# Kernel optimization log

Measured on AMD Instinct MI355X. Metric: run time of the kernel, lower is better.

## Reference

```python
import jax, jax.numpy as jnp
import numpy as np

N = 100000      # nodes
E = 1600000     # message-passing edges
P = 1000000     # prediction edges
DIN = 128       # node_in_channels
H = 128         # hidden_channels
DOUT = 64       # out_channels (node embedding)
EIN = 32        # edge_in_channels
EPS = 1e-5


def setup_inputs() -> dict:
    key = jax.random.key(0)
    ks = iter(jax.random.split(key, 48))
    nk = lambda: next(ks)
    rn = lambda shape: jax.random.normal(nk(), shape, dtype=jnp.float32)
    glorot = lambda shape: rn(shape) * (1.0 / np.sqrt(shape[-1]))
    inp = {
        "x": rn((N, DIN)),
        "edge_index": jax.random.randint(nk(), (2, E), 0, N),
        "pred_edge_index": jax.random.randint(nk(), (2, P), 0, N),
        "edge_features": rn((P, EIN)),
        # SAGEConv layer 1: lin_l (aggregated, with bias), lin_r (root, no bias)
        "sage1_Wl": glorot((H, DIN)), "sage1_bl": jnp.zeros((H,), jnp.float32), "sage1_Wr": glorot((H, DIN)),
        "bn1_g": jnp.ones((H,), jnp.float32), "bn1_b": jnp.zeros((H,), jnp.float32),
        "bn1_m": rn((H,)) * 0.1, "bn1_v": jnp.ones((H,), jnp.float32),
        # SAGEConv layer 2
        "sage2_Wl": glorot((DOUT, H)), "sage2_bl": jnp.zeros((DOUT,), jnp.float32), "sage2_Wr": glorot((DOUT, H)),
        # edge MLP: Linear(EIN, H//2) -> BN -> ReLU -> Linear(H//2, H//4)
        "edge_W1": glorot((H // 2, EIN)), "edge_b1": jnp.zeros((H // 2,), jnp.float32),
        "ebn_g": jnp.ones((H // 2,), jnp.float32), "ebn_b": jnp.zeros((H // 2,), jnp.float32),
        "ebn_m": rn((H // 2,)) * 0.1, "ebn_v": jnp.ones((H // 2,), jnp.float32),
        "edge_W2": glorot((H // 4, H // 2)), "edge_b2": jnp.zeros((H // 4,), jnp.float32),
        # predictor: Linear(2*DOUT+H//4, H) -> BN -> ReLU -> Linear(H, H//2) -> BN -> ReLU -> Linear(H//2, 1)
        "p_W1": glorot((H, 2 * DOUT + H // 4)), "p_b1": jnp.zeros((H,), jnp.float32),
        "pbn1_g": jnp.ones((H,), jnp.float32), "pbn1_b": jnp.zeros((H,), jnp.float32),
        "pbn1_m": rn((H,)) * 0.1, "pbn1_v": jnp.ones((H,), jnp.float32),
        "p_W2": glorot((H // 2, H)), "p_b2": jnp.zeros((H // 2,), jnp.float32),
        "pbn2_g": jnp.ones((H // 2,), jnp.float32), "pbn2_b": jnp.zeros((H // 2,), jnp.float32),
        "pbn2_m": rn((H // 2,)) * 0.1, "pbn2_v": jnp.ones((H // 2,), jnp.float32),
        "p_W3": glorot((1, H // 2)), "p_b3": jnp.zeros((1,), jnp.float32),
    }
    return inp


def _bn(h, g, b, m, v):
    # eval-mode BatchNorm1d with running stats
    return (h - m) * (g / jnp.sqrt(v + EPS)) + b


def _sage(h, src, dst, Wl, bl, Wr):
    # PyG SAGEConv (mean aggr): lin_l(mean of h[src] at dst) + lin_r(h)
    msg = jax.ops.segment_sum(h[src], dst, num_segments=N)        # [N, d]
    cnt = jax.ops.segment_sum(jnp.ones((src.shape[0],), h.dtype), dst, num_segments=N)
    agg = msg / jnp.maximum(cnt, 1.0)[:, None]
    return agg @ Wl.T + bl + h @ Wr.T


def reference(x, edge_index, pred_edge_index, edge_features,
              sage1_Wl, sage1_bl, sage1_Wr, bn1_g, bn1_b, bn1_m, bn1_v,
              sage2_Wl, sage2_bl, sage2_Wr,
              edge_W1, edge_b1, ebn_g, ebn_b, ebn_m, ebn_v, edge_W2, edge_b2,
              p_W1, p_b1, pbn1_g, pbn1_b, pbn1_m, pbn1_v,
              p_W2, p_b2, pbn2_g, pbn2_b, pbn2_m, pbn2_v, p_W3, p_b3):
    src, dst = edge_index[0], edge_index[1]
    # GraphSAGE encoder (eval mode: dropout off, BN running stats)
    h = _sage(x, src, dst, sage1_Wl, sage1_bl, sage1_Wr)
    h = jax.nn.relu(_bn(h, bn1_g, bn1_b, bn1_m, bn1_v))
    z = _sage(h, src, dst, sage2_Wl, sage2_bl, sage2_Wr)          # [N, DOUT]
    # edge-pair gather + concat
    combined = jnp.concatenate([z[pred_edge_index[0]], z[pred_edge_index[1]]], axis=-1)  # [P, 2*DOUT]
    # edge feature MLP
    e = edge_features @ edge_W1.T + edge_b1
    e = jax.nn.relu(_bn(e, ebn_g, ebn_b, ebn_m, ebn_v))
    e = e @ edge_W2.T + edge_b2                                   # [P, H//4]
    combined = jnp.concatenate([combined, e], axis=-1)            # [P, 2*DOUT + H//4]
    # predictor MLP
    u = combined @ p_W1.T + p_b1
    u = jax.nn.relu(_bn(u, pbn1_g, pbn1_b, pbn1_m, pbn1_v))
    u = u @ p_W2.T + p_b2
    u = jax.nn.relu(_bn(u, pbn2_g, pbn2_b, pbn2_m, pbn2_v))
    out = u @ p_W3.T + p_b3                                       # [P, 1]
    return out[:, 0]
```

## Files before the change

kernel.cpp:

```cpp
#include <hip/hip_runtime.h>

#define Nn 100000
#define Ee 1600000
#define Pp 1000000
#define EPSf 1e-5f

typedef _Float16 f16x8 __attribute__((ext_vector_type(8)));
typedef _Float16 f16x4 __attribute__((ext_vector_type(4)));
typedef _Float16 f16x2 __attribute__((ext_vector_type(2)));
typedef float f32x4 __attribute__((ext_vector_type(4)));

__device__ __forceinline__ float4 ld4(const float* p) { return *(const float4*)p; }

#define oW1l 0
#define oW1r 16384
#define oW2l 32768
#define oW2r 40960
#define oW1a 49152
#define oW1b 57344
#define oW1c 65536
#define oWe1 69632
#define oWe2 71680
#define oWp2 73728
#define W16_TOTAL 81920

#define BN_TOTAL 608

#define BSH 9
#define NB2 196
#define SCAP2 9216
#define ECHUNK 4096
#define NCHUNK ((Ee + ECHUNK - 1) / ECHUNK)

__global__ __launch_bounds__(256) void prep_kernel(
    const float* __restrict__ x,
    const float* __restrict__ s1Wl, const float* __restrict__ s1Wr,
    const float* __restrict__ s2Wl, const float* __restrict__ s2Wr,
    const float* __restrict__ pW1,  const float* __restrict__ eW1,
    const float* __restrict__ eW2,  const float* __restrict__ pW2,
    const float* __restrict__ eb1,
    const float* __restrict__ ebng, const float* __restrict__ ebnb,
    const float* __restrict__ ebnm, const float* __restrict__ ebnv,
    const float* __restrict__ eb2,
    const float* __restrict__ pb1,
    const float* __restrict__ p1g, const float* __restrict__ p1b,
    const float* __restrict__ p1m, const float* __restrict__ p1v,
    const float* __restrict__ pb2,
    const float* __restrict__ p2g, const float* __restrict__ p2b,
    const float* __restrict__ p2m, const float* __restrict__ p2v,
    const float* __restrict__ pW3,
    _Float16* __restrict__ w16, float* __restrict__ bnA,
    _Float16* __restrict__ x16) {
    int tid = blockIdx.x * 256 + threadIdx.x;
    if (tid < W16_TOTAL) {
        float v;
        if (tid < 16384)      v = s1Wl[tid];
        else if (tid < 32768) v = s1Wr[tid - 16384];
        else if (tid < 40960) v = s2Wl[tid - 32768];
        else if (tid < 49152) v = s2Wr[tid - 40960];
        else if (tid < 57344) { int l = tid - 49152; v = pW1[(l >> 6) * 160 + (l & 63)]; }
        else if (tid < 65536) { int l = tid - 57344; v = pW1[(l >> 6) * 160 + 64 + (l & 63)]; }
        else if (tid < 69632) { int l = tid - 65536; v = pW1[(l >> 5) * 160 + 128 + (l & 31)]; }
        else if (tid < 71680) v = eW1[tid - 69632];
        else if (tid < 73728) v = eW2[tid - 71680];
        else                  v = pW2[tid - 73728];
        w16[tid] = (_Float16)v;
    } else if (tid < W16_TOTAL + BN_TOTAL) {
        int b = tid - W16_TOTAL;
        float v;
        if (b < 64)       v = ebng[b] * rsqrtf(ebnv[b] + EPSf);
        else if (b < 128) { int c = b - 64;  float s = ebng[c] * rsqrtf(ebnv[c] + EPSf);
                            v = (eb1[c] - ebnm[c]) * s + ebnb[c]; }
        else if (b < 256) { int c = b - 128; v = p1g[c] * rsqrtf(p1v[c] + EPSf); }
        else if (b < 384) { int c = b - 256; float s = p1g[c] * rsqrtf(p1v[c] + EPSf);
                            v = (pb1[c] - p1m[c]) * s + p1b[c]; }
        else if (b < 448) { int c = b - 384; v = p2g[c] * rsqrtf(p2v[c] + EPSf); }
        else if (b < 512) { int c = b - 448; float s = p2g[c] * rsqrtf(p2v[c] + EPSf);
                            v = (pb2[c] - p2m[c]) * s + p2b[c]; }
        else if (b < 544) v = eb2[b - 512];
        else              v = pW3[b - 544];
        bnA[b] = v;
    }
    int stride = gridDim.x * 256;
    const int NV = Nn * 128 / 4;
    for (int i = tid; i < NV; i += stride) {
        float4 v = ((const float4*)x)[i];
        f16x4 h = {(_Float16)v.x, (_Float16)v.y, (_Float16)v.z, (_Float16)v.w};
        ((f16x4*)x16)[i] = h;
    }
}

__global__ __launch_bounds__(256) void bucketA_kernel(
    const int* __restrict__ src, const int* __restrict__ dst,
    unsigned* __restrict__ stage, unsigned* __restrict__ gcur) {
    __shared__ unsigned hist[NB2];
    __shared__ unsigned base[NB2];
    const int t = threadIdx.x;
    const int e0 = blockIdx.x * ECHUNK;
    for (int u = t; u < NB2; u += 256) hist[u] = 0u;
    __syncthreads();

    int sv[16], dv[16];
#pragma unroll
    for (int k = 0; k < 16; ++k) {
        int e = e0 + k * 256 + t;
        if (e < Ee) {
            sv[k] = src[e];
            dv[k] = dst[e];
            atomicAdd(&hist[dv[k] >> BSH], 1u);
        } else dv[k] = -1;
    }
    __syncthreads();
    for (int u = t; u < NB2; u += 256) {
        unsigned h = hist[u];
        base[u] = h ? atomicAdd(&gcur[u], h) : 0u;
        hist[u] = 0u;
    }
    __syncthreads();
#pragma unroll
    for (int k = 0; k < 16; ++k) {
        if (dv[k] >= 0) {
            int b = dv[k] >> BSH;
            unsigned p = atomicAdd(&hist[b], 1u);
            stage[(size_t)b * SCAP2 + base[b] + p] =
                ((unsigned)sv[k] << BSH) | (unsigned)(dv[k] & 511);
        }
    }
}

__global__ __launch_bounds__(256) void countC_kernel(
    const unsigned* __restrict__ stage, const unsigned* __restrict__ gcur,
    unsigned* __restrict__ deg) {
    __shared__ unsigned cnt[512];
    const int b = blockIdx.x;
    const int t = threadIdx.x;
    cnt[t] = 0u; cnt[t + 256] = 0u;
    __syncthreads();
    unsigned m = gcur[b];
    const unsigned* sp = stage + (size_t)b * SCAP2;
    for (unsigned i = t; i < m; i += 256)
        atomicAdd(&cnt[sp[i] & 511], 1u);
    __syncthreads();
    int n0 = b << BSH;
    if (n0 + t < Nn)       deg[n0 + t] = cnt[t];
    if (n0 + 256 + t < Nn) deg[n0 + 256 + t] = cnt[t + 256];
}

__global__ __launch_bounds__(1024) void scanA_kernel(const unsigned* __restrict__ deg,
                                                     unsigned* __restrict__ escan,
                                                     unsigned* __restrict__ bsum) {
    __shared__ unsigned s[1024];
    int t = threadIdx.x;
    int gid = blockIdx.x * 1024 + t;
    unsigned v = (gid < Nn) ? deg[gid] : 0u;
    s[t] = v;
    __syncthreads();
    for (int off = 1; off < 1024; off <<= 1) {
        unsigned u = (t >= off) ? s[t - off] : 0u;
        __syncthreads();
        s[t] += u;
        __syncthreads();
    }
    if (gid < Nn) escan[gid] = s[t] - v;
    if (t == 1023) bsum[blockIdx.x] = s[1023];
}

__global__ __launch_bounds__(128) void scanB_kernel(const unsigned* __restrict__ bsum,
                                                    unsigned* __restrict__ boff,
                                                    int nblk) {
    __shared__ unsigned s[128];
    int t = threadIdx.x;
    unsigned v = (t < nblk) ? bsum[t] : 0u;
    s[t] = v;
    __syncthreads();
    for (int off = 1; off < 128; off <<= 1) {
        unsigned u = (t >= off) ? s[t - off] : 0u;
        __syncthreads();
        s[t] += u;
        __syncthreads();
    }
    if (t < nblk) boff[t] = s[t] - v;
}

__global__ __launch_bounds__(1024) void scanC_kernel(const unsigned* __restrict__ escan,
                                                     const unsigned* __restrict__ boff,
                                                     int* __restrict__ rowptr) {
    int t = threadIdx.x;
    int gid = blockIdx.x * 1024 + t;
    if (gid < Nn) rowptr[gid] = (int)(escan[gid] + boff[blockIdx.x]);
    if (gid == 0) rowptr[Nn] = Ee;
}

__global__ __launch_bounds__(256) void scatterE_kernel(
    const unsigned* __restrict__ stage, const unsigned* __restrict__ gcur,
    const int* __restrict__ rowptr, int* __restrict__ elist) {
    __shared__ int lbase[512];
    __shared__ unsigned cur[512];
    const int b = blockIdx.x;
    const int t = threadIdx.x;
    const int n0 = b << BSH;
    lbase[t]       = (n0 + t < Nn)       ? rowptr[n0 + t]       : 0;
    lbase[t + 256] = (n0 + 256 + t < Nn) ? rowptr[n0 + 256 + t] : 0;
    cur[t] = 0u; cur[t + 256] = 0u;
    __syncthreads();
    unsigned m = gcur[b];
    const unsigned* sp = stage + (size_t)b * SCAP2;
    for (unsigned i = t; i < m; i += 256) {
        unsigned v = sp[i];
        int lid = v & 511;
        unsigned p = atomicAdd(&cur[lid], 1u);
        elist[lbase[lid] + p] = (int)(v >> BSH);
    }
}

template<int W>
__global__ __launch_bounds__(256, 8) void aggregate16_kernel(
    const _Float16* __restrict__ feat,
    const int* __restrict__ rowptr,
    const int* __restrict__ elist,
    _Float16* __restrict__ outp) {
    int node = (blockIdx.x * 256 + threadIdx.x) >> 6;
    int lane = threadIdx.x & 63;
    if (node >= Nn) return;
    constexpr int SEGS = W / 8;
    constexpr int RPI  = 64 / SEGS;
    const int r = lane / SEGS, c = lane % SEGS;
    int beg = rowptr[node], end = rowptr[node + 1];
    int n = end - beg;
    float acc[8];
#pragma unroll
    for (int k = 0; k < 8; ++k) acc[k] = 0.f;
    for (int c0 = 0; c0 < n; c0 += 64) {
        int m = min(64, n - c0);
        int se = (lane < m) ? elist[beg + c0 + lane] : 0;
        int iters = (m + RPI - 1) / RPI;
#pragma unroll 2
        for (int i = 0; i < iters; ++i) {
            int j = i * RPI + r;
            int s = __shfl(se, j);
            if (j < m) {
                f16x8 v = *(const f16x8*)(feat + (size_t)s * W + c * 8);
#pragma unroll
                for (int k = 0; k < 8; ++k) acc[k] += (float)v[k];
            }
        }
    }
#pragma unroll
    for (int k = 0; k < 8; ++k) {
#pragma unroll
        for (int off = SEGS; off < 64; off <<= 1)
            acc[k] += __shfl_xor(acc[k], off);
    }
    if (r == 0) {
        float inv = 1.0f / fmaxf((float)n, 1.0f);
        f16x8 o;
#pragma unroll
        for (int k = 0; k < 8; ++k) o[k] = (_Float16)(acc[k] * inv);
        *(f16x8*)(outp + (size_t)node * W + c * 8) = o;
    }
}

__global__ __launch_bounds__(256) void dense1_kernel(
    const _Float16* __restrict__ A1, const _Float16* __restrict__ A2,
    const _Float16* __restrict__ W1, const _Float16* __restrict__ W2,
    const float* __restrict__ lb,
    const float* __restrict__ bng, const float* __restrict__ bnb,
    const float* __restrict__ bnm, const float* __restrict__ bnv,
    _Float16* __restrict__ out) {
    const int t = threadIdx.x;
    const int w = t >> 6, lane = t & 63;
    const int lrow = lane & 15, lq = lane >> 4;
    const int row0 = blockIdx.x * 64 + w * 16;
    const int ld = min(row0 + lrow, Nn - 1);

    f16x8 a1[4], a2[4];
#pragma unroll
    for (int i = 0; i < 4; ++i) {
        a1[i] = *(const f16x8*)(A1 + (size_t)ld * 128 + i * 32 + lq * 8);
        a2[i] = *(const f16x8*)(A2 + (size_t)ld * 128 + i * 32 + lq * 8);
    }
#pragma unroll
    for (int nt = 0; nt < 8; ++nt) {
        const _Float16* w1r = W1 + (size_t)(nt * 16 + lrow) * 128;
        const _Float16* w2r = W2 + (size_t)(nt * 16 + lrow) * 128;
        f32x4 c = {0.f, 0.f, 0.f, 0.f};
#pragma unroll
        for (int i = 0; i < 4; ++i) {
            c = __builtin_amdgcn_mfma_f32_16x16x32_f16(a1[i], *(const f16x8*)(w1r + i * 32 + lq * 8), c, 0, 0, 0);
            c = __builtin_amdgcn_mfma_f32_16x16x32_f16(a2[i], *(const f16x8*)(w2r + i * 32 + lq * 8), c, 0, 0, 0);
        }
        int cc = nt * 16 + lrow;
        float s = bng[cc] * rsqrtf(bnv[cc] + EPSf);
        float h = (lb[cc] - bnm[cc]) * s + bnb[cc];
#pragma unroll
        for (int r = 0; r < 4; ++r) {
            int gr = row0 + lq * 4 + r;
            if (gr < Nn)
                out[(size_t)gr * 128 + cc] = (_Float16)fmaxf(c[r] * s + h, 0.f);
        }
    }
}

__global__ __launch_bounds__(256) void gemmY_kernel(
    const _Float16* __restrict__ A, const _Float16* __restrict__ W,
    _Float16* __restrict__ out) {
    const int t = threadIdx.x;
    const int w = t >> 6, lane = t & 63;
    const int lrow = lane & 15, lq = lane >> 4;
    const int row0 = blockIdx.x * 64 + w * 16;
    const int ld = min(row0 + lrow, Nn - 1);
    f16x8 a[4];
#pragma unroll
    for (int i = 0; i < 4; ++i)
        a[i] = *(const f16x8*)(A + (size_t)ld * 128 + i * 32 + lq * 8);
#pragma unroll
    for (int nt = 0; nt < 4; ++nt) {
        const _Float16* wr = W + (size_t)(nt * 16 + lrow) * 128;
        f32x4 c = {0.f, 0.f, 0.f, 0.f};
#pragma unroll
        for (int i = 0; i < 4; ++i)
            c = __builtin_amdgcn_mfma_f32_16x16x32_f16(a[i], *(const f16x8*)(wr + i * 32 + lq * 8), c, 0, 0, 0);
        int cc = nt * 16 + lrow;
#pragma unroll
        for (int r = 0; r < 4; ++r) {
            int gr = row0 + lq * 4 + r;
            if (gr < Nn) out[(size_t)gr * 64 + cc] = (_Float16)c[r];
        }
    }
}

__global__ __launch_bounds__(256) void dense2b_kernel(
    const _Float16* __restrict__ aggY, const _Float16* __restrict__ A2,
    const _Float16* __restrict__ W2, const float* __restrict__ lb,
    _Float16* __restrict__ out) {
    const int t = threadIdx.x;
    const int w = t >> 6, lane = t & 63;
    const int lrow = lane & 15, lq = lane >> 4;
    const int row0 = blockIdx.x * 64 + w * 16;
    const int ld = min(row0 + lrow, Nn - 1);
    f16x8 a[4];
#pragma unroll
    for (int i = 0; i < 4; ++i)
        a[i] = *(const f16x8*)(A2 + (size_t)ld * 128 + i * 32 + lq * 8);
#pragma unroll
    for (int nt = 0; nt < 4; ++nt) {
        const _Float16* wr = W2 + (size_t)(nt * 16 + lrow) * 128;
        f32x4 c = {0.f, 0.f, 0.f, 0.f};
#pragma unroll
        for (int i = 0; i < 4; ++i)
            c = __builtin_amdgcn_mfma_f32_16x16x32_f16(a[i], *(const f16x8*)(wr + i * 32 + lq * 8), c, 0, 0, 0);
        int cc = nt * 16 + lrow;
        float b = lb[cc];
#pragma unroll
        for (int r = 0; r < 4; ++r) {
            int gr = row0 + lq * 4 + r;
            if (gr < Nn) {
                float g = (float)aggY[(size_t)gr * 64 + cc];
                out[(size_t)gr * 64 + cc] = (_Float16)(c[r] + g + b);
            }
        }
    }
}

__global__ __launch_bounds__(256) void emlp_kernel(
    const float* __restrict__ ef,
    const _Float16* __restrict__ w16,
    const float* __restrict__ bnA,
    _Float16* __restrict__ e2out) {
    __shared__ __align__(16) _Float16 E1[64 * 72];
    const int t = threadIdx.x;
    const int lane = t & 63, w = t >> 6;
    const int lrow = lane & 15, lq = lane >> 4;
    const int e0 = blockIdx.x * 64 + w * 16;
    const int erow = w * 16 + lrow;

    const float* src = ef + (size_t)(e0 + lrow) * 32 + lq * 8;
    float4 f0 = ld4(src), f1 = ld4(src + 4);
    f16x8 bf = {(_Float16)f0.x, (_Float16)f0.y, (_Float16)f0.z, (_Float16)f0.w,
                (_Float16)f1.x, (_Float16)f1.y, (_Float16)f1.z, (_Float16)f1.w};

#pragma unroll
    for (int nt = 0; nt < 4; ++nt) {
        f16x8 wf = *(const f16x8*)(w16 + oWe1 + (nt * 16 + lrow) * 32 + lq * 8);
        f32x4 c = {0.f, 0.f, 0.f, 0.f};
        c = __builtin_amdgcn_mfma_f32_16x16x32_f16(wf, bf, c, 0, 0, 0);
        int cb = nt * 16 + lq * 4;
        float4 s = *(const float4*)(bnA + cb);
        float4 h = *(const float4*)(bnA + 64 + cb);
        f16x4 o;
        o[0] = (_Float16)fmaxf(c[0] * s.x + h.x, 0.f);
        o[1] = (_Float16)fmaxf(c[1] * s.y + h.y, 0.f);
        o[2] = (_Float16)fmaxf(c[2] * s.z + h.z, 0.f);
        o[3] = (_Float16)fmaxf(c[3] * s.w + h.w, 0.f);
        *(f16x4*)(E1 + erow * 72 + cb) = o;
    }
    f16x8 a0 = *(const f16x8*)(E1 + erow * 72 + lq * 8);
    f16x8 a1 = *(const f16x8*)(E1 + erow * 72 + 32 + lq * 8);
#pragma unroll
    for (int nt = 0; nt < 2; ++nt) {
        f16x8 b0 = *(const f16x8*)(w16 + oWe2 + (nt * 16 + lrow) * 64 + lq * 8);
        f16x8 b1 = *(const f16x8*)(w16 + oWe2 + (nt * 16 + lrow) * 64 + 32 + lq * 8);
        f32x4 c = {0.f, 0.f, 0.f, 0.f};
        c = __builtin_amdgcn_mfma_f32_16x16x32_f16(b0, a0, c, 0, 0, 0);
        c = __builtin_amdgcn_mfma_f32_16x16x32_f16(b1, a1, c, 0, 0, 0);
        int cb = nt * 16 + lq * 4;
        float4 bias = *(const float4*)(bnA + 512 + cb);
        f16x4 o;
        o[0] = (_Float16)(c[0] + bias.x);
        o[1] = (_Float16)(c[1] + bias.y);
        o[2] = (_Float16)(c[2] + bias.z);
        o[3] = (_Float16)(c[3] + bias.w);
        *(f16x4*)(e2out + (size_t)(e0 + lrow) * 32 + cb) = o;
    }
}

#define EPB 256
#define NT  ((Pp + EPB - 1) / EPB)
#define EGRID 256

#define oL_W1a 0
#define oL_W1b 18432
#define oL_W1c 36864
#define oL_Wp2 47104
#define oL_BN  64512
#define oL_ZU  66304
#define SMEM_BYTES 135936

__global__ __launch_bounds__(1024, 4) void edge_kernel(
    const int* __restrict__ pe,
    const _Float16* __restrict__ e2,
    const _Float16* __restrict__ z,
    const _Float16* __restrict__ w16,
    const float* __restrict__ bnA,
    const float* __restrict__ pb3,
    float* __restrict__ out) {
    __shared__ __align__(16) unsigned char smem[SMEM_BYTES];
    _Float16* LW1a = (_Float16*)(smem + oL_W1a);
    _Float16* LW1b = (_Float16*)(smem + oL_W1b);
    _Float16* LW1c = (_Float16*)(smem + oL_W1c);
    _Float16* LWp2 = (_Float16*)(smem + oL_Wp2);
    float*    LBN  = (float*)(smem + oL_BN);
    _Float16* ZU   = (_Float16*)(smem + oL_ZU);

    const float* bn2s = LBN;        const float* bn2h = LBN + 128;
    const float* bn3s = LBN + 256;  const float* bn3h = LBN + 320;
    const float* wp3g = LBN + 384;

    const int t = threadIdx.x;
    const int lane = t & 63;
    const int w = t >> 6;
    const int m0 = w * 16;
    const int lrow = lane & 15;
    const int lq = lane >> 4;
    const float pb3v = pb3[0];

    auto load_idx = [&](int tl, int& ia, int& ib) {
        int e = min(tl * EPB + m0 + lrow, Pp - 1);
        ia = pe[e];
        ib = pe[Pp + e];
    };
    auto gather = [&](int tl, int ia, int ib, f16x8* F) {
        F[0] = *(const f16x8*)(z + (size_t)ia * 64 + lq * 8);
        F[1] = *(const f16x8*)(z + (size_t)ia * 64 + 32 + lq * 8);
        F[2] = *(const f16x8*)(z + (size_t)ib * 64 + lq * 8);
        F[3] = *(const f16x8*)(z + (size_t)ib * 64 + 32 + lq * 8);
        int e = min(tl * EPB + m0 + lrow, Pp - 1);
        F[4] = *(const f16x8*)(e2 + (size_t)e * 32 + lq * 8);
    };

    int tile = blockIdx.x;
    int ia1, ib1;
    {
        int ia0, ib0;
        load_idx(tile, ia0, ib0);
        load_idx(tile + EGRID, ia1, ib1);
        f16x8 F[5];
        gather(tile, ia0, ib0, F);

        { int r = t >> 3, s = t & 7;
          *(f16x8*)(LW1a + r * 72 + s * 8) = *(const f16x8*)(w16 + oW1a + r * 64 + s * 8);
          *(f16x8*)(LW1b + r * 72 + s * 8) = *(const f16x8*)(w16 + oW1b + r * 64 + s * 8); }
        if (t < 512) { int r = t >> 2, s = t & 3;
          *(f16x8*)(LW1c + r * 40 + s * 8) = *(const f16x8*)(w16 + oW1c + r * 32 + s * 8); }
        { int r = t >> 4, s = t & 15;
          *(f16x8*)(LWp2 + r * 136 + s * 8) = *(const f16x8*)(w16 + oWp2 + r * 128 + s * 8); }
        if (t < 384) LBN[t] = bnA[128 + t];
        else if (t < 448) LBN[t] = bnA[544 + (t - 384)];
        __syncthreads();

        const int erow = m0 + lrow;
        const int zr = erow * 136;
        for (; tile < NT; tile += EGRID) {
            f16x8 G[5];
            gather(tile + EGRID, ia1, ib1, G);
            int ia2, ib2;
            load_idx(tile + 2 * EGRID, ia2, ib2);

            const bool act = (tile * EPB + m0) < Pp;
            if (act) {
                __builtin_amdgcn_s_setprio(1);
#pragma unroll
                for (int nt = 0; nt < 8; ++nt) {
                    const _Float16* wa = LW1a + (nt * 16 + lrow) * 72;
                    const _Float16* wb = LW1b + (nt * 16 + lrow) * 72;
                    const _Float16* wc = LW1c + (nt * 16 + lrow) * 40;
                    f32x4 c = {0.f, 0.f, 0.f, 0.f};
                    c = __builtin_amdgcn_mfma_f32_16x16x32_f16(*(const f16x8*)(wa + lq * 8),      F[0], c, 0, 0, 0);
                    c = __builtin_amdgcn_mfma_f32_16x16x32_f16(*(const f16x8*)(wa + 32 + lq * 8), F[1], c, 0, 0, 0);
                    c = __builtin_amdgcn_mfma_f32_16x16x32_f16(*(const f16x8*)(wb + lq * 8),      F[2], c, 0, 0, 0);
                    c = __builtin_amdgcn_mfma_f32_16x16x32_f16(*(const f16x8*)(wb + 32 + lq * 8), F[3], c, 0, 0, 0);
                    c = __builtin_amdgcn_mfma_f32_16x16x32_f16(*(const f16x8*)(wc + lq * 8),      F[4], c, 0, 0, 0);
                    int cb = nt * 16 + lq * 4;
                    float4 s = *(const float4*)(bn2s + cb);
                    float4 h = *(const float4*)(bn2h + cb);
                    f16x4 o;
                    o[0] = (_Float16)fmaxf(c[0] * s.x + h.x, 0.f);
                    o[1] = (_Float16)fmaxf(c[1] * s.y + h.y, 0.f);
                    o[2] = (_Float16)fmaxf(c[2] * s.z + h.z, 0.f);
                    o[3] = (_Float16)fmaxf(c[3] * s.w + h.w, 0.f);
                    *(f16x4*)(ZU + zr + cb) = o;
                }
                __builtin_amdgcn_s_setprio(0);
                {
                    f16x8 a0 = *(const f16x8*)(ZU + zr + 0  + lq * 8);
                    f16x8 a1 = *(const f16x8*)(ZU + zr + 32 + lq * 8);
                    f16x8 a2 = *(const f16x8*)(ZU + zr + 64 + lq * 8);
                    f16x8 a3 = *(const f16x8*)(ZU + zr + 96 + lq * 8);
                    float acc = 0.f;
                    __builtin_amdgcn_s_setprio(1);
#pragma unroll
                    for (int nt = 0; nt < 4; ++nt) {
                        const _Float16* wr = LWp2 + (nt * 16 + lrow) * 136 + lq * 8;
                        f32x4 c = {0.f, 0.f, 0.f, 0.f};
                        c = __builtin_amdgcn_mfma_f32_16x16x32_f16(*(const f16x8*)(wr + 0),  a0, c, 0, 0, 0);
                        c = __builtin_amdgcn_mfma_f32_16x16x32_f16(*(const f16x8*)(wr + 32), a1, c, 0, 0, 0);
                        c = __builtin_amdgcn_mfma_f32_16x16x32_f16(*(const f16x8*)(wr + 64), a2, c, 0, 0, 0);
                        c = __builtin_amdgcn_mfma_f32_16x16x32_f16(*(const f16x8*)(wr + 96), a3, c, 0, 0, 0);
                        int cb = nt * 16 + lq * 4;
                        float4 s  = *(const float4*)(bn3s + cb);
                        float4 h  = *(const float4*)(bn3h + cb);
                        float4 w3 = *(const float4*)(wp3g + cb);
                        acc += fmaxf(c[0] * s.x + h.x, 0.f) * w3.x;
                        acc += fmaxf(c[1] * s.y + h.y, 0.f) * w3.y;
                        acc += fmaxf(c[2] * s.z + h.z, 0.f) * w3.z;
                        acc += fmaxf(c[3] * s.w + h.w, 0.f) * w3.w;
                    }
                    __builtin_amdgcn_s_setprio(0);
                    acc += __shfl_xor(acc, 16);
                    acc += __shfl_xor(acc, 32);
                    if (lane < 16) out[tile * EPB + m0 + lane] = acc + pb3v;
                }
            }
#pragma unroll
            for (int i = 0; i < 5; ++i) F[i] = G[i];
            ia1 = ia2; ib1 = ib2;
        }
    }
}

extern "C" void kernel_launch(void* const* d_in, const int* in_sizes, int n_in,
                              void* d_out, int out_size, void* d_ws, size_t ws_size,
                              hipStream_t stream) {
    const float* x    = (const float*)d_in[0];
    const int*   eidx = (const int*)d_in[1];
    const int*   pe   = (const int*)d_in[2];
    const float* ef   = (const float*)d_in[3];
    const float* s1Wl = (const float*)d_in[4];
    const float* s1bl = (const float*)d_in[5];
    const float* s1Wr = (const float*)d_in[6];
    const float* bn1g = (const float*)d_in[7];
    const float* bn1b = (const float*)d_in[8];
    const float* bn1m = (const float*)d_in[9];
    const float* bn1v = (const float*)d_in[10];
    const float* s2Wl = (const float*)d_in[11];
    const float* s2bl = (const float*)d_in[12];
    const float* s2Wr = (const float*)d_in[13];
    const float* eW1  = (const float*)d_in[14];
    const float* eb1  = (const float*)d_in[15];
    const float* ebng = (const float*)d_in[16];
    const float* ebnb = (const float*)d_in[17];
    const float* ebnm = (const float*)d_in[18];
    const float* ebnv = (const float*)d_in[19];
    const float* eW2  = (const float*)d_in[20];
    const float* eb2  = (const float*)d_in[21];
    const float* pW1  = (const float*)d_in[22];
    const float* pb1  = (const float*)d_in[23];
    const float* p1g  = (const float*)d_in[24];
    const float* p1b  = (const float*)d_in[25];
    const float* p1m  = (const float*)d_in[26];
    const float* p1v  = (const float*)d_in[27];
    const float* pW2  = (const float*)d_in[28];
    const float* pb2  = (const float*)d_in[29];
    const float* p2g  = (const float*)d_in[30];
    const float* p2b  = (const float*)d_in[31];
    const float* p2m  = (const float*)d_in[32];
    const float* p2v  = (const float*)d_in[33];
    const float* pW3  = (const float*)d_in[34];
    const float* pb3  = (const float*)d_in[35];
    float* out = (float*)d_out;

    char* wk = (char*)d_ws;
    auto carve = [&](size_t bytes) {
        char* p = wk;
        wk += (bytes + 255) & ~(size_t)255;
        return p;
    };
    unsigned*  deg    = (unsigned*)carve((size_t)Nn * 4);
    unsigned*  gcur   = (unsigned*)carve((size_t)256 * 4);
    int*       rowptr = (int*)carve((size_t)(Nn + 1) * 4);
    int*       elist  = (int*)carve((size_t)Ee * 4);
    unsigned*  escan  = (unsigned*)carve((size_t)Nn * 4);
    unsigned*  bsum   = (unsigned*)carve(128 * 4);
    unsigned*  boff   = (unsigned*)carve(128 * 4);
    _Float16*  w16    = (_Float16*)carve((size_t)W16_TOTAL * 2);
    float*     bnA    = (float*)carve((size_t)BN_TOTAL * 4);
    _Float16*  bufX   = (_Float16*)carve((size_t)Nn * 128 * 2);
    _Float16*  bufA   = (_Float16*)carve((size_t)Nn * 128 * 2);
    _Float16*  bufH   = (_Float16*)carve((size_t)Nn * 128 * 2);
    _Float16*  e2buf  = (_Float16*)carve((size_t)Pp * 32 * 2);
    _Float16*  bufY   = bufX;
    _Float16*  bufZ   = bufX + (size_t)Nn * 64;
    _Float16*  bufAy  = bufA;
    unsigned*  stage  = (unsigned*)bufH;

    const int* e_src = eidx;
    const int* e_dst = eidx + Ee;
    const int SBLK = (Nn + 1023) / 1024;

    hipMemsetAsync(gcur, 0, 256 * 4, stream);

    prep_kernel<<<800, 256, 0, stream>>>(x, s1Wl, s1Wr, s2Wl, s2Wr, pW1, eW1, eW2, pW2,
                                         eb1, ebng, ebnb, ebnm, ebnv, eb2,
                                         pb1, p1g, p1b, p1m, p1v,
                                         pb2, p2g, p2b, p2m, p2v, pW3,
                                         w16, bnA, bufX);
    emlp_kernel<<<Pp / 64, 256, 0, stream>>>(ef, w16, bnA, e2buf);

    bucketA_kernel<<<NCHUNK, 256, 0, stream>>>(e_src, e_dst, stage, gcur);
    countC_kernel<<<NB2, 256, 0, stream>>>(stage, gcur, deg);
    scanA_kernel<<<SBLK, 1024, 0, stream>>>(deg, escan, bsum);
    scanB_kernel<<<1, 128, 0, stream>>>(bsum, boff, SBLK);
    scanC_kernel<<<SBLK, 1024, 0, stream>>>(escan, boff, rowptr);
    scatterE_kernel<<<NB2, 256, 0, stream>>>(stage, gcur, rowptr, elist);

    aggregate16_kernel<128><<<Nn / 4, 256, 0, stream>>>(bufX, rowptr, elist, bufA);
    dense1_kernel<<<(Nn + 63) / 64, 256, 0, stream>>>(
        bufA, bufX, w16 + oW1l, w16 + oW1r, s1bl, bn1g, bn1b, bn1m, bn1v, bufH);

    gemmY_kernel<<<(Nn + 63) / 64, 256, 0, stream>>>(bufH, w16 + oW2l, bufY);
    aggregate16_kernel<64><<<Nn / 4, 256, 0, stream>>>(bufY, rowptr, elist, bufAy);
    dense2b_kernel<<<(Nn + 63) / 64, 256, 0, stream>>>(
        bufAy, bufH, w16 + oW2r, s2bl, bufZ);

    edge_kernel<<<EGRID, 1024, 0, stream>>>(pe, e2buf, bufZ, w16, bnA, pb3, out);
}
```

Before: 676.6 us.

## Fold BN scales into predictor weights, interleave layer-2 MFMA, shrink LDS for occupancy

Folds the predictor BatchNorm scales into the fp16 W1/W2 weights during preprocessing, so the edge kernel only adds a shift. The second predictor layer is interleaved with the first: each 32-column chunk of the hidden activations goes through a small swizzled per-wave LDS buffer and straight into the layer-2 MFMAs, instead of staging the full 128-wide row. This cuts LDS to about 80KB, so launch bounds rise to 8 blocks and the grid to 512. The explicit two-deep register prefetch of gathers is dropped in favour of higher occupancy, which risks exposing more gather latency per wave.

```diff
diff --git a/kernel.cpp b/kernel.cpp
--- a/kernel.cpp
+++ b/kernel.cpp
@@ -58,12 +58,16 @@
         else if (tid < 32768) v = s1Wr[tid - 16384];
         else if (tid < 40960) v = s2Wl[tid - 32768];
         else if (tid < 49152) v = s2Wr[tid - 40960];
-        else if (tid < 57344) { int l = tid - 49152; v = pW1[(l >> 6) * 160 + (l & 63)]; }
-        else if (tid < 65536) { int l = tid - 57344; v = pW1[(l >> 6) * 160 + 64 + (l & 63)]; }
-        else if (tid < 69632) { int l = tid - 65536; v = pW1[(l >> 5) * 160 + 128 + (l & 31)]; }
+        else if (tid < 57344) { int l = tid - 49152; int r = l >> 6;
+                                v = pW1[r * 160 + (l & 63)] * (p1g[r] * rsqrtf(p1v[r] + EPSf)); }
+        else if (tid < 65536) { int l = tid - 57344; int r = l >> 6;
+                                v = pW1[r * 160 + 64 + (l & 63)] * (p1g[r] * rsqrtf(p1v[r] + EPSf)); }
+        else if (tid < 69632) { int l = tid - 65536; int r = l >> 5;
+                                v = pW1[r * 160 + 128 + (l & 31)] * (p1g[r] * rsqrtf(p1v[r] + EPSf)); }
         else if (tid < 71680) v = eW1[tid - 69632];
         else if (tid < 73728) v = eW2[tid - 71680];
-        else                  v = pW2[tid - 73728];
+        else                  { int l = tid - 73728; int r = l >> 7;
+                                v = pW2[l] * (p2g[r] * rsqrtf(p2v[r] + EPSf)); }
         w16[tid] = (_Float16)v;
     } else if (tid < W16_TOTAL + BN_TOTAL) {
         int b = tid - W16_TOTAL;
@@ -416,17 +420,16 @@
 
 #define EPB 256
 #define NT  ((Pp + EPB - 1) / EPB)
-#define EGRID 256
+#define EGRID 512
 
 #define oL_W1a 0
 #define oL_W1b 18432
 #define oL_W1c 36864
 #define oL_Wp2 47104
-#define oL_BN  64512
-#define oL_ZU  66304
-#define SMEM_BYTES 135936
-
-__global__ __launch_bounds__(1024, 4) void edge_kernel(
+#define oL_ZU  64512
+#define SMEM_BYTES 80896
+
+__global__ __launch_bounds__(1024, 8) void edge_kernel(
     const int* __restrict__ pe,
     const _Float16* __restrict__ e2,
     const _Float16* __restrict__ z,
@@ -439,12 +442,7 @@
     _Float16* LW1b = (_Float16*)(smem + oL_W1b);
     _Float16* LW1c = (_Float16*)(smem + oL_W1c);
     _Float16* LWp2 = (_Float16*)(smem + oL_Wp2);
-    float*    LBN  = (float*)(smem + oL_BN);
-    _Float16* ZU   = (_Float16*)(smem + oL_ZU);
-
-    const float* bn2s = LBN;        const float* bn2h = LBN + 128;
-    const float* bn3s = LBN + 256;  const float* bn3h = LBN + 320;
-    const float* wp3g = LBN + 384;
+    unsigned char* ZU = smem + oL_ZU;
 
     const int t = threadIdx.x;
     const int lane = t & 63;
@@ -454,106 +452,85 @@
     const int lq = lane >> 4;
     const float pb3v = pb3[0];
 
-    auto load_idx = [&](int tl, int& ia, int& ib) {
-        int e = min(tl * EPB + m0 + lrow, Pp - 1);
-        ia = pe[e];
-        ib = pe[Pp + e];
-    };
-    auto gather = [&](int tl, int ia, int ib, f16x8* F) {
-        F[0] = *(const f16x8*)(z + (size_t)ia * 64 + lq * 8);
-        F[1] = *(const f16x8*)(z + (size_t)ia * 64 + 32 + lq * 8);
-        F[2] = *(const f16x8*)(z + (size_t)ib * 64 + lq * 8);
-        F[3] = *(const f16x8*)(z + (size_t)ib * 64 + 32 + lq * 8);
-        int e = min(tl * EPB + m0 + lrow, Pp - 1);
-        F[4] = *(const f16x8*)(e2 + (size_t)e * 32 + lq * 8);
-    };
+    { int r = t >> 3, s = t & 7;
+      *(f16x8*)(LW1a + r * 72 + s * 8) = *(const f16x8*)(w16 + oW1a + r * 64 + s * 8);
+      *(f16x8*)(LW1b + r * 72 + s * 8) = *(const f16x8*)(w16 + oW1b + r * 64 + s * 8); }
+    if (t < 512) { int r = t >> 2, s = t & 3;
+      *(f16x8*)(LW1c + r * 40 + s * 8) = *(const f16x8*)(w16 + oW1c + r * 32 + s * 8); }
+    { int r = t >> 4, s = t & 15;
+      *(f16x8*)(LWp2 + r * 136 + s * 8) = *(const f16x8*)(w16 + oWp2 + r * 128 + s * 8); }
+    __syncthreads();
+
+    const int erow = m0 + lrow;
+    unsigned char* zrow = ZU + erow * 64;
+    const int zswz = (erow & 3) << 4;
 
     int tile = blockIdx.x;
-    int ia1, ib1;
-    {
-        int ia0, ib0;
-        load_idx(tile, ia0, ib0);
-        load_idx(tile + EGRID, ia1, ib1);
-        f16x8 F[5];
-        gather(tile, ia0, ib0, F);
-
-        { int r = t >> 3, s = t & 7;
-          *(f16x8*)(LW1a + r * 72 + s * 8) = *(const f16x8*)(w16 + oW1a + r * 64 + s * 8);
-          *(f16x8*)(LW1b + r * 72 + s * 8) = *(const f16x8*)(w16 + oW1b + r * 64 + s * 8); }
-        if (t < 512) { int r = t >> 2, s = t & 3;
-          *(f16x8*)(LW1c + r * 40 + s * 8) = *(const f16x8*)(w16 + oW1c + r * 32 + s * 8); }
-        { int r = t >> 4, s = t & 15;
-          *(f16x8*)(LWp2 + r * 136 + s * 8) = *(const f16x8*)(w16 + oWp2 + r * 128 + s * 8); }
-        if (t < 384) LBN[t] = bnA[128 + t];
-        else if (t < 448) LBN[t] = bnA[544 + (t - 384)];
-        __syncthreads();
-
-        const int erow = m0 + lrow;
-        const int zr = erow * 136;
-        for (; tile < NT; tile += EGRID) {
-            f16x8 G[5];
-            gather(tile + EGRID, ia1, ib1, G);
-            int ia2, ib2;
-            load_idx(tile + 2 * EGRID, ia2, ib2);
-
-            const bool act = (tile * EPB + m0) < Pp;
-            if (act) {
-                __builtin_amdgcn_s_setprio(1);
-#pragma unroll
-                for (int nt = 0; nt < 8; ++nt) {
+    int ia, ib;
+    { int e = min(tile * EPB + m0 + lrow, Pp - 1);
+      ia = pe[e]; ib = pe[Pp + e]; }
+
+    for (; tile < NT; tile += EGRID) {
+        const int e_cur = tile * EPB + m0;
+        f16x8 F0 = *(const f16x8*)(z + (size_t)ia * 64 + lq * 8);
+        f16x8 F1 = *(const f16x8*)(z + (size_t)ia * 64 + 32 + lq * 8);
+        f16x8 F2 = *(const f16x8*)(z + (size_t)ib * 64 + lq * 8);
+        f16x8 F3 = *(const f16x8*)(z + (size_t)ib * 64 + 32 + lq * 8);
+        f16x8 F4;
+        { int e = min(e_cur + lrow, Pp - 1);
+          F4 = *(const f16x8*)(e2 + (size_t)e * 32 + lq * 8); }
+        { int tl = tile + EGRID;
+          if (tl < NT) { int e = min(tl * EPB + m0 + lrow, Pp - 1);
+                         ia = pe[e]; ib = pe[Pp + e]; } }
+
+        if (e_cur < Pp) {
+            f32x4 c6[4] = {{0.f,0.f,0.f,0.f},{0.f,0.f,0.f,0.f},
+                           {0.f,0.f,0.f,0.f},{0.f,0.f,0.f,0.f}};
+            __builtin_amdgcn_s_setprio(1);
+#pragma unroll
+            for (int p = 0; p < 4; ++p) {
+#pragma unroll
+                for (int h2 = 0; h2 < 2; ++h2) {
+                    const int nt = 2 * p + h2;
                     const _Float16* wa = LW1a + (nt * 16 + lrow) * 72;
                     const _Float16* wb = LW1b + (nt * 16 + lrow) * 72;
                     const _Float16* wc = LW1c + (nt * 16 + lrow) * 40;
                     f32x4 c = {0.f, 0.f, 0.f, 0.f};
-                    c = __builtin_amdgcn_mfma_f32_16x16x32_f16(*(const f16x8*)(wa + lq * 8),      F[0], c, 0, 0, 0);
-                    c = __builtin_amdgcn_mfma_f32_16x16x32_f16(*(const f16x8*)(wa + 32 + lq * 8), F[1], c, 0, 0, 0);
-                    c = __builtin_amdgcn_mfma_f32_16x16x32_f16(*(const f16x8*)(wb + lq * 8),      F[2], c, 0, 0, 0);
-                    c = __builtin_amdgcn_mfma_f32_16x16x32_f16(*(const f16x8*)(wb + 32 + lq * 8), F[3], c, 0, 0, 0);
-                    c = __builtin_amdgcn_mfma_f32_16x16x32_f16(*(const f16x8*)(wc + lq * 8),      F[4], c, 0, 0, 0);
-                    int cb = nt * 16 + lq * 4;
-                    float4 s = *(const float4*)(bn2s + cb);
-                    float4 h = *(const float4*)(bn2h + cb);
+                    c = __builtin_amdgcn_mfma_f32_16x16x32_f16(*(const f16x8*)(wa + lq * 8),      F0, c, 0, 0, 0);
+                    c = __builtin_amdgcn_mfma_f32_16x16x32_f16(*(const f16x8*)(wa + 32 + lq * 8), F1, c, 0, 0, 0);
+                    c = __builtin_amdgcn_mfma_f32_16x16x32_f16(*(const f16x8*)(wb + lq * 8),      F2, c, 0, 0, 0);
+                    c = __builtin_amdgcn_mfma_f32_16x16x32_f16(*(const f16x8*)(wb + 32 + lq * 8), F3, c, 0, 0, 0);
+                    c = __builtin_amdgcn_mfma_f32_16x16x32_f16(*(const f16x8*)(wc + lq * 8),      F4, c, 0, 0, 0);
+                    float4 hh = *(const float4*)(bnA + 256 + nt * 16 + lq * 4);
                     f16x4 o;
-                    o[0] = (_Float16)fmaxf(c[0] * s.x + h.x, 0.f);
-                    o[1] = (_Float16)fmaxf(c[1] * s.y + h.y, 0.f);
-                    o[2] = (_Float16)fmaxf(c[2] * s.z + h.z, 0.f);
-                    o[3] = (_Float16)fmaxf(c[3] * s.w + h.w, 0.f);
-                    *(f16x4*)(ZU + zr + cb) = o;
+                    o[0] = (_Float16)fmaxf(c[0] + hh.x, 0.f);
+                    o[1] = (_Float16)fmaxf(c[1] + hh.y, 0.f);
+                    o[2] = (_Float16)fmaxf(c[2] + hh.z, 0.f);
+                    o[3] = (_Float16)fmaxf(c[3] + hh.w, 0.f);
+                    *(f16x4*)(zrow + ((h2 * 32 + lq * 8) ^ zswz)) = o;
                 }
-                __builtin_amdgcn_s_setprio(0);
-                {
-                    f16x8 a0 = *(const f16x8*)(ZU + zr + 0  + lq * 8);
-                    f16x8 a1 = *(const f16x8*)(ZU + zr + 32 + lq * 8);
-                    f16x8 a2 = *(const f16x8*)(ZU + zr + 64 + lq * 8);
-                    f16x8 a3 = *(const f16x8*)(ZU + zr + 96 + lq * 8);
-                    float acc = 0.f;
-                    __builtin_amdgcn_s_setprio(1);
-#pragma unroll
-                    for (int nt = 0; nt < 4; ++nt) {
-                        const _Float16* wr = LWp2 + (nt * 16 + lrow) * 136 + lq * 8;
-                        f32x4 c = {0.f, 0.f, 0.f, 0.f};
-                        c = __builtin_amdgcn_mfma_f32_16x16x32_f16(*(const f16x8*)(wr + 0),  a0, c, 0, 0, 0);
-                        c = __builtin_amdgcn_mfma_f32_16x16x32_f16(*(const f16x8*)(wr + 32), a1, c, 0, 0, 0);
-                        c = __builtin_amdgcn_mfma_f32_16x16x32_f16(*(const f16x8*)(wr + 64), a2, c, 0, 0, 0);
-                        c = __builtin_amdgcn_mfma_f32_16x16x32_f16(*(const f16x8*)(wr + 96), a3, c, 0, 0, 0);
-                        int cb = nt * 16 + lq * 4;
-                        float4 s  = *(const float4*)(bn3s + cb);
-                        float4 h  = *(const float4*)(bn3h + cb);
-                        float4 w3 = *(const float4*)(wp3g + cb);
-                        acc += fmaxf(c[0] * s.x + h.x, 0.f) * w3.x;
-                        acc += fmaxf(c[1] * s.y + h.y, 0.f) * w3.y;
-                        acc += fmaxf(c[2] * s.z + h.z, 0.f) * w3.z;
-                        acc += fmaxf(c[3] * s.w + h.w, 0.f) * w3.w;
-                    }
-                    __builtin_amdgcn_s_setprio(0);
-                    acc += __shfl_xor(acc, 16);
-                    acc += __shfl_xor(acc, 32);
-                    if (lane < 16) out[tile * EPB + m0 + lane] = acc + pb3v;
+                f16x8 a = *(const f16x8*)(zrow + ((lq * 16) ^ zswz));
+#pragma unroll
+                for (int nt2 = 0; nt2 < 4; ++nt2) {
+                    const _Float16* wr = LWp2 + (nt2 * 16 + lrow) * 136 + p * 32 + lq * 8;
+                    c6[nt2] = __builtin_amdgcn_mfma_f32_16x16x32_f16(*(const f16x8*)(wr), a, c6[nt2], 0, 0, 0);
                 }
             }
-#pragma unroll
-            for (int i = 0; i < 5; ++i) F[i] = G[i];
-            ia1 = ia2; ib1 = ib2;
+            __builtin_amdgcn_s_setprio(0);
+            float acc = 0.f;
+#pragma unroll
+            for (int nt2 = 0; nt2 < 4; ++nt2) {
+                int cb = nt2 * 16 + lq * 4;
+                float4 h3 = *(const float4*)(bnA + 448 + cb);
+                float4 w3 = *(const float4*)(bnA + 544 + cb);
+                acc += fmaxf(c6[nt2][0] + h3.x, 0.f) * w3.x;
+                acc += fmaxf(c6[nt2][1] + h3.y, 0.f) * w3.y;
+                acc += fmaxf(c6[nt2][2] + h3.z, 0.f) * w3.z;
+                acc += fmaxf(c6[nt2][3] + h3.w, 0.f) * w3.w;
+            }
+            acc += __shfl_xor(acc, 16);
+            acc += __shfl_xor(acc, 32);
+            if (lane < 16) out[e_cur + lane] = acc + pb3v;
         }
     }
 }
```

Result: no change. 687.0 us (+1.5%).
